# Kernel tuning notes

Measured on AMD Instinct MI355X. Metric: run time of the kernel, lower is better.

Reference implementation:

```python
import jax, jax.numpy as jnp
import numpy as np

N_NODES = 100000
N_EDGES = 1600000
N_GRAPHS = 256
BN_EPS = 1e-5


def _graph_conv(x, src, dst, ew, w_rel, b_rel, w_root):
    # PyG GraphConv: aggregate add of edge_weight * x[src] at dst, then dense transform
    msg = x[src] * ew[:, None]                      # [E, F] gathered messages
    agg = jax.ops.segment_sum(msg, dst, num_segments=N_NODES)  # [N, F]
    return agg @ w_rel + b_rel + x @ w_root


def _bn_eval(x, g, b, m, v):
    return (x - m) * jax.lax.rsqrt(v + BN_EPS) * g + b


def setup_inputs() -> dict:
    key = jax.random.key(0)
    ks = jax.random.split(key, 32)
    d = {}
    d["x"] = jax.random.normal(ks[0], (N_NODES, 29), dtype=jnp.float32)
    d["edge_index"] = jax.random.randint(ks[1], (2, N_EDGES), 0, N_NODES, dtype=jnp.int64)
    d["edge_weight"] = jax.random.uniform(ks[2], (N_EDGES,), dtype=jnp.float32)
    d["batch"] = jnp.sort(jax.random.randint(ks[3], (N_NODES,), 0, N_GRAPHS, dtype=jnp.int64))
    dims = [(29, 256), (256, 128), (128, 64), (64, 32)]
    for i, (fi, fo) in enumerate(dims, start=1):
        s = 1.0 / np.sqrt(fi)
        d[f"w{i}_rel"] = jax.random.uniform(ks[4 + 3 * i], (fi, fo), minval=-s, maxval=s, dtype=jnp.float32)
        d[f"b{i}_rel"] = jax.random.uniform(ks[5 + 3 * i], (fo,), minval=-s, maxval=s, dtype=jnp.float32)
        d[f"w{i}_root"] = jax.random.uniform(ks[6 + 3 * i], (fi, fo), minval=-s, maxval=s, dtype=jnp.float32)
    for j, c in enumerate([128, 64, 32], start=1):
        kb = jax.random.split(jax.random.fold_in(key, 100 + j), 4)
        d[f"bn{j}_g"] = 1.0 + 0.1 * jax.random.normal(kb[0], (c,), dtype=jnp.float32)
        d[f"bn{j}_b"] = 0.1 * jax.random.normal(kb[1], (c,), dtype=jnp.float32)
        d[f"bn{j}_m"] = 0.1 * jax.random.normal(kb[2], (c,), dtype=jnp.float32)
        d[f"bn{j}_v"] = 0.5 + jax.random.uniform(kb[3], (c,), dtype=jnp.float32)
    s = 1.0 / np.sqrt(32.0)
    d["fc_w"] = jax.random.uniform(ks[30], (32, 1), minval=-s, maxval=s, dtype=jnp.float32)
    d["fc_b"] = jax.random.uniform(ks[31], (1,), minval=-s, maxval=s, dtype=jnp.float32)
    return d


def reference(x, edge_index, edge_weight, batch,
              w1_rel, b1_rel, w1_root, w2_rel, b2_rel, w2_root,
              w3_rel, b3_rel, w3_root, w4_rel, b4_rel, w4_root,
              bn1_g, bn1_b, bn1_m, bn1_v,
              bn2_g, bn2_b, bn2_m, bn2_v,
              bn3_g, bn3_b, bn3_m, bn3_v,
              fc_w, fc_b):
    src, dst = edge_index[0], edge_index[1]
    h = jax.nn.relu(_graph_conv(x, src, dst, edge_weight, w1_rel, b1_rel, w1_root))
    h = _graph_conv(h, src, dst, edge_weight, w2_rel, b2_rel, w2_root)
    h = jax.nn.relu(_bn_eval(h, bn1_g, bn1_b, bn1_m, bn1_v))
    h = _graph_conv(h, src, dst, edge_weight, w3_rel, b3_rel, w3_root)
    h = jax.nn.relu(_bn_eval(h, bn2_g, bn2_b, bn2_m, bn2_v))
    h = _graph_conv(h, src, dst, edge_weight, w4_rel, b4_rel, w4_root)
    h = jax.nn.relu(_bn_eval(h, bn3_g, bn3_b, bn3_m, bn3_v))
    # global mean pool over graphs
    sums = jax.ops.segment_sum(h, batch, num_segments=N_GRAPHS)        # [G, 32]
    cnts = jax.ops.segment_sum(jnp.ones((h.shape[0],), h.dtype), batch, num_segments=N_GRAPHS)
    pooled = sums / jnp.maximum(cnts, 1.0)[:, None]
    return jax.nn.sigmoid(pooled @ fc_w + fc_b)                         # [G, 1]
```

## Files before the change

kernel.cpp:

```cpp
#include <hip/hip_runtime.h>
#include <math.h>

#define N_NODES 100000
#define N_EDGES 1600000
#define N_GRAPHS 256
#define BN_EPS 1e-5f

__global__ void hist_kernel(const int* __restrict__ ei, int* __restrict__ deg) {
    int e = blockIdx.x * blockDim.x + threadIdx.x;
    if (e < N_EDGES) atomicAdd(&deg[ei[N_EDGES + e]], 1);
}

__global__ void scan1_kernel(const int* __restrict__ deg, int* __restrict__ rowptr,
                             int* __restrict__ bsum) {
    __shared__ int s[256];
    int tid = threadIdx.x;
    int i = blockIdx.x * 256 + tid;
    int v = (i < N_NODES) ? deg[i] : 0;
    s[tid] = v; __syncthreads();
    for (int off = 1; off < 256; off <<= 1) {
        int t = (tid >= off) ? s[tid - off] : 0; __syncthreads();
        s[tid] += t; __syncthreads();
    }
    if (i < N_NODES) rowptr[i] = s[tid] - v;
    if (tid == 255) bsum[blockIdx.x] = s[255];
}

__global__ void scan2_kernel(int* bsum, int nb) {
    __shared__ int s[512];
    int tid = threadIdx.x;
    int v = (tid < nb) ? bsum[tid] : 0;
    s[tid] = v; __syncthreads();
    for (int off = 1; off < 512; off <<= 1) {
        int t = (tid >= off) ? s[tid - off] : 0; __syncthreads();
        s[tid] += t; __syncthreads();
    }
    if (tid < nb) bsum[tid] = s[tid] - v;
}

__global__ void scan3_kernel(int* __restrict__ rowptr, const int* __restrict__ bsum) {
    int i = blockIdx.x * 256 + threadIdx.x;
    if (i < N_NODES) rowptr[i] += bsum[blockIdx.x];
    if (i == 0) rowptr[N_NODES] = N_EDGES;
}

__global__ void scatter_kernel(const int* __restrict__ ei, const float* __restrict__ ew,
                               const int* __restrict__ rowptr, int* __restrict__ cnt,
                               int* __restrict__ ssrc, float* __restrict__ swt) {
    int e = blockIdx.x * blockDim.x + threadIdx.x;
    if (e >= N_EDGES) return;
    int dst = ei[N_EDGES + e];
    int pos = rowptr[dst] + atomicAdd(&cnt[dst], 1);
    ssrc[pos] = ei[e];
    swt[pos] = ew[e];
}

__global__ void bnprep_kernel(const float* __restrict__ v1, const float* __restrict__ v2,
                              const float* __restrict__ v3, float* __restrict__ rs) {
    int t = threadIdx.x;
    if (t < 128) rs[t] = 1.0f / sqrtf(v1[t] + BN_EPS);
    if (t < 64)  rs[128 + t] = 1.0f / sqrtf(v2[t] + BN_EPS);
    if (t < 32)  rs[192 + t] = 1.0f / sqrtf(v3[t] + BN_EPS);
}

__global__ void starts_kernel(const int* __restrict__ batch, int* __restrict__ starts) {
    int i = blockIdx.x * 256 + threadIdx.x;
    if (i >= N_NODES) return;
    int b = batch[i];
    int bp = (i == 0) ? -1 : batch[i - 1];
    for (int g = bp + 1; g <= b; ++g) starts[g] = i;
    if (i == N_NODES - 1)
        for (int g = b + 1; g <= N_GRAPHS; ++g) starts[g] = N_NODES;
}

__global__ __launch_bounds__(256) void pad_x_kernel(const float* __restrict__ x,
                                                    float* __restrict__ xp) {
    int i = blockIdx.x * 256 + threadIdx.x;
    if (i >= N_NODES * 32) return;
    int n = i >> 5, c = i & 31;
    xp[i] = (c < 29) ? x[n * 29 + c] : 0.f;
}

__global__ __launch_bounds__(256) void agg_x_kernel(const float* __restrict__ xp,
        const int* __restrict__ rowptr, const int* __restrict__ ssrc,
        const float* __restrict__ swt, float* __restrict__ agg) {
    int tid = threadIdx.x;
    int node = blockIdx.x * 32 + (tid >> 3);
    int c = (tid & 7) * 4;
    int e0 = rowptr[node], e1 = rowptr[node + 1];
    float4 acc = {0.f, 0.f, 0.f, 0.f};
    int e = e0;
    for (; e < e1 && (e & 3); ++e) {
        int s0 = ssrc[e]; float w0 = swt[e];
        float4 y0 = *(const float4*)&xp[(size_t)s0 * 32 + c];
        acc.x = fmaf(w0, y0.x, acc.x); acc.y = fmaf(w0, y0.y, acc.y);
        acc.z = fmaf(w0, y0.z, acc.z); acc.w = fmaf(w0, y0.w, acc.w);
    }
    for (; e + 4 <= e1; e += 4) {
        int4   s4 = *(const int4*)&ssrc[e];
        float4 w4 = *(const float4*)&swt[e];
        float4 y0 = *(const float4*)&xp[(size_t)s4.x * 32 + c];
        float4 y1 = *(const float4*)&xp[(size_t)s4.y * 32 + c];
        float4 y2 = *(const float4*)&xp[(size_t)s4.z * 32 + c];
        float4 y3 = *(const float4*)&xp[(size_t)s4.w * 32 + c];
        acc.x = fmaf(w4.x, y0.x, acc.x); acc.y = fmaf(w4.x, y0.y, acc.y);
        acc.z = fmaf(w4.x, y0.z, acc.z); acc.w = fmaf(w4.x, y0.w, acc.w);
        acc.x = fmaf(w4.y, y1.x, acc.x); acc.y = fmaf(w4.y, y1.y, acc.y);
        acc.z = fmaf(w4.y, y1.z, acc.z); acc.w = fmaf(w4.y, y1.w, acc.w);
        acc.x = fmaf(w4.z, y2.x, acc.x); acc.y = fmaf(w4.z, y2.y, acc.y);
        acc.z = fmaf(w4.z, y2.z, acc.z); acc.w = fmaf(w4.z, y2.w, acc.w);
        acc.x = fmaf(w4.w, y3.x, acc.x); acc.y = fmaf(w4.w, y3.y, acc.y);
        acc.z = fmaf(w4.w, y3.z, acc.z); acc.w = fmaf(w4.w, y3.w, acc.w);
    }
    for (; e < e1; ++e) {
        int s0 = ssrc[e]; float w0 = swt[e];
        float4 y0 = *(const float4*)&xp[(size_t)s0 * 32 + c];
        acc.x = fmaf(w0, y0.x, acc.x); acc.y = fmaf(w0, y0.y, acc.y);
        acc.z = fmaf(w0, y0.z, acc.z); acc.w = fmaf(w0, y0.w, acc.w);
    }
    *(float4*)&agg[(size_t)node * 32 + c] = acc;
}

__global__ __launch_bounds__(256) void dense1_kernel(const float* __restrict__ agg,
        const float* __restrict__ xp, const float* __restrict__ wrel,
        const float* __restrict__ wroot, const float* __restrict__ bias,
        float* __restrict__ out) {
    __shared__ float sA[32 * 32];
    __shared__ float sX[32 * 32];
    int tid = threadIdx.x;
    int node0 = blockIdx.x * 32;
    ((float4*)sA)[tid] = ((const float4*)(agg + (size_t)node0 * 32))[tid];
    ((float4*)sX)[tid] = ((const float4*)(xp + (size_t)node0 * 32))[tid];
    __syncthreads();
    int ct = tid & 63;
    int mg = tid >> 6;
    int c0 = ct * 4;
    float acc[8][4];
#pragma unroll
    for (int m = 0; m < 8; m++)
#pragma unroll
        for (int j = 0; j < 4; j++) acc[m][j] = 0.f;
    for (int k0 = 0; k0 < 28; k0 += 4) {
        float4 wr[4], wo[4];
#pragma unroll
        for (int j = 0; j < 4; j++) {
            wr[j] = *(const float4*)&wrel[(k0 + j) * 256 + c0];
            wo[j] = *(const float4*)&wroot[(k0 + j) * 256 + c0];
        }
#pragma unroll
        for (int m = 0; m < 8; m++) {
            float4 av = *(const float4*)&sA[(mg * 8 + m) * 32 + k0];
            float4 xv = *(const float4*)&sX[(mg * 8 + m) * 32 + k0];
            float as[4] = {av.x, av.y, av.z, av.w};
            float xs[4] = {xv.x, xv.y, xv.z, xv.w};
#pragma unroll
            for (int j = 0; j < 4; j++) {
                acc[m][0] = fmaf(as[j], wr[j].x, fmaf(xs[j], wo[j].x, acc[m][0]));
                acc[m][1] = fmaf(as[j], wr[j].y, fmaf(xs[j], wo[j].y, acc[m][1]));
                acc[m][2] = fmaf(as[j], wr[j].z, fmaf(xs[j], wo[j].z, acc[m][2]));
                acc[m][3] = fmaf(as[j], wr[j].w, fmaf(xs[j], wo[j].w, acc[m][3]));
            }
        }
    }
    {
        float4 wr = *(const float4*)&wrel[28 * 256 + c0];
        float4 wo = *(const float4*)&wroot[28 * 256 + c0];
#pragma unroll
        for (int m = 0; m < 8; m++) {
            float sa = sA[(mg * 8 + m) * 32 + 28];
            float sx = sX[(mg * 8 + m) * 32 + 28];
            acc[m][0] = fmaf(sa, wr.x, fmaf(sx, wo.x, acc[m][0]));
            acc[m][1] = fmaf(sa, wr.y, fmaf(sx, wo.y, acc[m][1]));
            acc[m][2] = fmaf(sa, wr.z, fmaf(sx, wo.z, acc[m][2]));
            acc[m][3] = fmaf(sa, wr.w, fmaf(sx, wo.w, acc[m][3]));
        }
    }
    float4 b4 = *(const float4*)&bias[c0];
#pragma unroll
    for (int m = 0; m < 8; m++) {
        int row = node0 + mg * 8 + m;
        float4 o;
        o.x = fmaxf(acc[m][0] + b4.x, 0.f);
        o.y = fmaxf(acc[m][1] + b4.y, 0.f);
        o.z = fmaxf(acc[m][2] + b4.z, 0.f);
        o.w = fmaxf(acc[m][3] + b4.w, 0.f);
        *(float4*)&out[(size_t)row * 256 + c0] = o;
    }
}

template <int K, int F, int RPM, int KC>
__global__ __launch_bounds__(256) void gemm_dual_kernel(const float* __restrict__ in,
        const float* __restrict__ wA, const float* __restrict__ wB,
        float* __restrict__ outA, float* __restrict__ outB) {
    constexpr int NT = 256;
    constexpr int CPT = 8;
    constexpr int CQ = CPT / 4;
    constexpr int NCT = 2 * F / CPT;
    constexpr int MG = NT / NCT;
    constexpr int ROWS = MG * RPM;
    constexpr int KC4 = KC / 4;
    __shared__ float s[ROWS * KC];
    int tid = threadIdx.x;
    size_t node0 = (size_t)blockIdx.x * ROWS;
    int ct = tid % NCT;
    int mg = tid / NCT;
    int c0 = ct * CPT;
    const float* W;
    float* OUT;
    int cc;
    if (c0 < F) { W = wA; OUT = outA; cc = c0; }
    else        { W = wB; OUT = outB; cc = c0 - F; }
    float acc[RPM][CPT];
#pragma unroll
    for (int m = 0; m < RPM; m++)
#pragma unroll
        for (int j = 0; j < CPT; j++) acc[m][j] = 0.f;
    const float* srow = s + (size_t)(mg * RPM) * KC;
    for (int kb = 0; kb < K; kb += KC) {
        __syncthreads();
        for (int idx = tid; idx < ROWS * KC4; idx += NT) {
            int rr = idx / KC4;
            int c4 = idx % KC4;
            *(float4*)&s[rr * KC + c4 * 4] =
                *(const float4*)&in[(node0 + rr) * K + kb + c4 * 4];
        }
        __syncthreads();
        for (int k0 = 0; k0 < KC; k0 += 4) {
            float4 wv[4][CQ];
#pragma unroll
            for (int j = 0; j < 4; j++)
#pragma unroll
                for (int q = 0; q < CQ; q++)
                    wv[j][q] = *(const float4*)&W[(kb + k0 + j) * F + cc + q * 4];
#pragma unroll
            for (int m = 0; m < RPM; m++) {
                float4 av = *(const float4*)&srow[m * KC + k0];
                float as[4] = {av.x, av.y, av.z, av.w};
#pragma unroll
                for (int j = 0; j < 4; j++) {
#pragma unroll
                    for (int q = 0; q < CQ; q++) {
                        acc[m][q * 4 + 0] = fmaf(as[j], wv[j][q].x, acc[m][q * 4 + 0]);
                        acc[m][q * 4 + 1] = fmaf(as[j], wv[j][q].y, acc[m][q * 4 + 1]);
                        acc[m][q * 4 + 2] = fmaf(as[j], wv[j][q].z, acc[m][q * 4 + 2]);
                        acc[m][q * 4 + 3] = fmaf(as[j], wv[j][q].w, acc[m][q * 4 + 3]);
                    }
                }
            }
        }
    }
#pragma unroll
    for (int m = 0; m < RPM; m++) {
        size_t row = node0 + mg * RPM + m;
#pragma unroll
        for (int q = 0; q < CQ; q++) {
            float4 o = {acc[m][q * 4 + 0], acc[m][q * 4 + 1],
                        acc[m][q * 4 + 2], acc[m][q * 4 + 3]};
            *(float4*)&OUT[row * F + cc + q * 4] = o;
        }
    }
}

template <int F>
__global__ __launch_bounds__(256) void combine_kernel(const float* __restrict__ y,
        const float* __restrict__ r, const int* __restrict__ rowptr,
        const int* __restrict__ ssrc, const float* __restrict__ swt,
        const float* __restrict__ bias, const float* __restrict__ bg,
        const float* __restrict__ bb, const float* __restrict__ bm,
        const float* __restrict__ rs, float* __restrict__ h) {
    constexpr int TPN = F / 4;
    int tid = threadIdx.x;
    int node = blockIdx.x * (256 / TPN) + tid / TPN;
    int c = (tid % TPN) * 4;
    int e0 = rowptr[node], e1 = rowptr[node + 1];
    float4 acc = {0.f, 0.f, 0.f, 0.f};
    int e = e0;
    for (; e < e1 && (e & 3); ++e) {
        int s0 = ssrc[e]; float w0 = swt[e];
        float4 y0 = *(const float4*)&y[(size_t)s0 * F + c];
        acc.x = fmaf(w0, y0.x, acc.x); acc.y = fmaf(w0, y0.y, acc.y);
        acc.z = fmaf(w0, y0.z, acc.z); acc.w = fmaf(w0, y0.w, acc.w);
    }
    for (; e + 4 <= e1; e += 4) {
        int4   s4 = *(const int4*)&ssrc[e];
        float4 w4 = *(const float4*)&swt[e];
        float4 y0 = *(const float4*)&y[(size_t)s4.x * F + c];
        float4 y1 = *(const float4*)&y[(size_t)s4.y * F + c];
        float4 y2 = *(const float4*)&y[(size_t)s4.z * F + c];
        float4 y3 = *(const float4*)&y[(size_t)s4.w * F + c];
        acc.x = fmaf(w4.x, y0.x, acc.x); acc.y = fmaf(w4.x, y0.y, acc.y);
        acc.z = fmaf(w4.x, y0.z, acc.z); acc.w = fmaf(w4.x, y0.w, acc.w);
        acc.x = fmaf(w4.y, y1.x, acc.x); acc.y = fmaf(w4.y, y1.y, acc.y);
        acc.z = fmaf(w4.y, y1.z, acc.z); acc.w = fmaf(w4.y, y1.w, acc.w);
        acc.x = fmaf(w4.z, y2.x, acc.x); acc.y = fmaf(w4.z, y2.y, acc.y);
        acc.z = fmaf(w4.z, y2.z, acc.z); acc.w = fmaf(w4.z, y2.w, acc.w);
        acc.x = fmaf(w4.w, y3.x, acc.x); acc.y = fmaf(w4.w, y3.y, acc.y);
        acc.z = fmaf(w4.w, y3.z, acc.z); acc.w = fmaf(w4.w, y3.w, acc.w);
    }
    for (; e < e1; ++e) {
        int s0 = ssrc[e]; float w0 = swt[e];
        float4 y0 = *(const float4*)&y[(size_t)s0 * F + c];
        acc.x = fmaf(w0, y0.x, acc.x); acc.y = fmaf(w0, y0.y, acc.y);
        acc.z = fmaf(w0, y0.z, acc.z); acc.w = fmaf(w0, y0.w, acc.w);
    }
    float4 bi = *(const float4*)&bias[c];
    float4 rv = *(const float4*)&r[(size_t)node * F + c];
    float4 mu = *(const float4*)&bm[c];
    float4 rq = *(const float4*)&rs[c];
    float4 gm = *(const float4*)&bg[c];
    float4 bt = *(const float4*)&bb[c];
    float4 o;
    o.x = fmaxf((acc.x + bi.x + rv.x - mu.x) * rq.x * gm.x + bt.x, 0.f);
    o.y = fmaxf((acc.y + bi.y + rv.y - mu.y) * rq.y * gm.y + bt.y, 0.f);
    o.z = fmaxf((acc.z + bi.z + rv.z - mu.z) * rq.z * gm.z + bt.z, 0.f);
    o.w = fmaxf((acc.w + bi.w + rv.w - mu.w) * rq.w * gm.w + bt.w, 0.f);
    *(float4*)&h[(size_t)node * F + c] = o;
}

__global__ __launch_bounds__(256) void pool_fc_kernel(const float* __restrict__ h4,
        const int* __restrict__ starts, const float* __restrict__ fcw,
        const float* __restrict__ fcb, float* __restrict__ out) {
    int g = blockIdx.x;
    int tid = threadIdx.x;
    int i0 = starts[g], i1 = starts[g + 1];
    int ch = tid & 31, part = tid >> 5;
    float sum = 0.f;
    for (int i = i0 + part; i < i1; i += 8) sum += h4[(size_t)i * 32 + ch];
    __shared__ float sm[8][32];
    sm[part][ch] = sum;
    __syncthreads();
    if (tid < 32) {
        float tot = 0.f;
        for (int p = 0; p < 8; p++) tot += sm[p][tid];
        float cnt = (float)(i1 - i0);
        float mean = tot / fmaxf(cnt, 1.0f);
        sm[0][tid] = mean * fcw[tid];
    }
    __syncthreads();
    if (tid == 0) {
        float z = 0.f;
        for (int c = 0; c < 32; c++) z += sm[0][c];
        z += fcb[0];
        out[g] = 1.0f / (1.0f + expf(-z));
    }
}

extern "C" void kernel_launch(void* const* d_in, const int* in_sizes, int n_in,
                              void* d_out, int out_size, void* d_ws, size_t ws_size,
                              hipStream_t stream) {
    (void)in_sizes; (void)n_in; (void)out_size; (void)ws_size;
    const float* x       = (const float*)d_in[0];
    const int*   ei      = (const int*)d_in[1];
    const float* ew      = (const float*)d_in[2];
    const int*   batch   = (const int*)d_in[3];
    const float* w1_rel  = (const float*)d_in[4];
    const float* b1      = (const float*)d_in[5];
    const float* w1_root = (const float*)d_in[6];
    const float* w2_rel  = (const float*)d_in[7];
    const float* b2      = (const float*)d_in[8];
    const float* w2_root = (const float*)d_in[9];
    const float* w3_rel  = (const float*)d_in[10];
    const float* b3      = (const float*)d_in[11];
    const float* w3_root = (const float*)d_in[12];
    const float* w4_rel  = (const float*)d_in[13];
    const float* b4      = (const float*)d_in[14];
    const float* w4_root = (const float*)d_in[15];
    const float* bn1_g = (const float*)d_in[16];
    const float* bn1_b = (const float*)d_in[17];
    const float* bn1_m = (const float*)d_in[18];
    const float* bn2_g = (const float*)d_in[20];
    const float* bn2_b = (const float*)d_in[21];
    const float* bn2_m = (const float*)d_in[22];
    const float* bn3_g = (const float*)d_in[24];
    const float* bn3_b = (const float*)d_in[25];
    const float* bn3_m = (const float*)d_in[26];
    const float* fc_w = (const float*)d_in[28];
    const float* fc_b = (const float*)d_in[29];

    char* ws = (char*)d_ws;
    int*   rowptr = (int*)(ws + 0);
    int*   cnt    = (int*)(ws + (1ull << 20));
    int*   bsum   = (int*)(ws + (2ull << 20));
    float* rs     = (float*)(ws + (2ull << 20) + (64ull << 10));
    int*   starts = (int*)(ws + (2ull << 20) + (128ull << 10));
    int*   ssrc   = (int*)(ws + (4ull << 20));
    float* swt    = (float*)(ws + (11ull << 20));
    float* bufA   = (float*)(ws + (18ull << 20));
    float* bufB   = (float*)(ws + (122ull << 20));
    float* bufC   = (float*)(ws + (174ull << 20));
    float* xp   = bufB;
    float* agg1 = bufC;

    hipMemsetAsync(cnt, 0, N_NODES * 4, stream);
    hist_kernel<<<6250, 256, 0, stream>>>(ei, cnt);
    scan1_kernel<<<391, 256, 0, stream>>>(cnt, rowptr, bsum);
    scan2_kernel<<<1, 512, 0, stream>>>(bsum, 391);
    scan3_kernel<<<391, 256, 0, stream>>>(rowptr, bsum);
    hipMemsetAsync(cnt, 0, N_NODES * 4, stream);
    scatter_kernel<<<6250, 256, 0, stream>>>(ei, ew, rowptr, cnt, ssrc, swt);
    bnprep_kernel<<<1, 128, 0, stream>>>((const float*)d_in[19], (const float*)d_in[23],
                                         (const float*)d_in[27], rs);
    starts_kernel<<<391, 256, 0, stream>>>(batch, starts);

    pad_x_kernel<<<12500, 256, 0, stream>>>(x, xp);
    agg_x_kernel<<<3125, 256, 0, stream>>>(xp, rowptr, ssrc, swt, agg1);
    dense1_kernel<<<3125, 256, 0, stream>>>(agg1, xp, w1_rel, w1_root, b1, bufA);

    gemm_dual_kernel<256, 128, 8, 64><<<1563, 256, 0, stream>>>(bufA, w2_rel, w2_root, bufB, bufC);
    combine_kernel<128><<<12500, 256, 0, stream>>>(bufB, bufC, rowptr, ssrc, swt,
                                                   b2, bn1_g, bn1_b, bn1_m, rs, bufC);

    gemm_dual_kernel<128, 64, 4, 64><<<1563, 256, 0, stream>>>(bufC, w3_rel, w3_root, bufB, bufA);
    combine_kernel<64><<<6250, 256, 0, stream>>>(bufB, bufA, rowptr, ssrc, swt,
                                                 b3, bn2_g, bn2_b, bn2_m, rs + 128, bufA);

    gemm_dual_kernel<64, 32, 4, 32><<<782, 256, 0, stream>>>(bufA, w4_rel, w4_root, bufB, bufC);
    combine_kernel<32><<<3125, 256, 0, stream>>>(bufB, bufC, rowptr, ssrc, swt,
                                                 b4, bn3_g, bn3_b, bn3_m, rs + 192, bufC);

    pool_fc_kernel<<<N_GRAPHS, 256, 0, stream>>>(bufC, starts, fc_w, fc_b, (float*)d_out);
}
```

Measured before the change: 859.6 us.

## Double-buffer shared tiles and prefetch weights in dual GEMM kernel

The dual GEMM kernel now stages input tiles through two shared-memory buffers, loading the next K-chunk into registers while computing the current one, and prefetches the next weight rows into a second register set. Each thread now computes 4 output columns instead of 8, with rows per thread raised to keep the tile covering the same nodes. The aim is to hide global-load latency and remove one barrier per chunk. In exchange it uses more shared memory and staging registers, which may lower occupancy.

Measured after the change: 816.0 us. 5.1% less time.

```diff
diff --git a/kernel.cpp b/kernel.cpp
--- a/kernel.cpp
+++ b/kernel.cpp
@@ -193,71 +193,102 @@
         const float* __restrict__ wA, const float* __restrict__ wB,
         float* __restrict__ outA, float* __restrict__ outB) {
     constexpr int NT = 256;
-    constexpr int CPT = 8;
-    constexpr int CQ = CPT / 4;
-    constexpr int NCT = 2 * F / CPT;
+    constexpr int NCT = F / 2;
     constexpr int MG = NT / NCT;
     constexpr int ROWS = MG * RPM;
     constexpr int KC4 = KC / 4;
-    __shared__ float s[ROWS * KC];
+    constexpr int LPT = (ROWS * KC4) / NT;
+    __shared__ float sbuf[2][ROWS * KC];
     int tid = threadIdx.x;
     size_t node0 = (size_t)blockIdx.x * ROWS;
     int ct = tid % NCT;
     int mg = tid / NCT;
-    int c0 = ct * CPT;
+    int c0 = ct * 4;
     const float* W;
     float* OUT;
     int cc;
     if (c0 < F) { W = wA; OUT = outA; cc = c0; }
     else        { W = wB; OUT = outB; cc = c0 - F; }
-    float acc[RPM][CPT];
+    float acc[RPM][4];
 #pragma unroll
     for (int m = 0; m < RPM; m++)
 #pragma unroll
-        for (int j = 0; j < CPT; j++) acc[m][j] = 0.f;
-    const float* srow = s + (size_t)(mg * RPM) * KC;
+        for (int j = 0; j < 4; j++) acc[m][j] = 0.f;
+
+#pragma unroll
+    for (int i = 0; i < LPT; i++) {
+        int idx = tid + i * NT;
+        int rr = idx / KC4, c4 = idx % KC4;
+        *(float4*)&sbuf[0][rr * KC + c4 * 4] =
+            *(const float4*)&in[(node0 + rr) * K + c4 * 4];
+    }
+    float4 wv[2][4];
+#pragma unroll
+    for (int j = 0; j < 4; j++) wv[0][j] = *(const float4*)&W[j * F + cc];
+    __syncthreads();
+
+    int cur = 0;
+#pragma unroll 1
     for (int kb = 0; kb < K; kb += KC) {
-        __syncthreads();
-        for (int idx = tid; idx < ROWS * KC4; idx += NT) {
-            int rr = idx / KC4;
-            int c4 = idx % KC4;
-            *(float4*)&s[rr * KC + c4 * 4] =
-                *(const float4*)&in[(node0 + rr) * K + kb + c4 * 4];
-        }
-        __syncthreads();
+        const bool more = (kb + KC < K);
+        float4 st[LPT];
+        if (more) {
+#pragma unroll
+            for (int i = 0; i < LPT; i++) {
+                int idx = tid + i * NT;
+                int rr = idx / KC4, c4 = idx % KC4;
+                st[i] = *(const float4*)&in[(node0 + rr) * K + (kb + KC) + c4 * 4];
+            }
+        }
+        const float* srow = &sbuf[cur][0] + (size_t)(mg * RPM) * KC;
+#pragma unroll
         for (int k0 = 0; k0 < KC; k0 += 4) {
-            float4 wv[4][CQ];
-#pragma unroll
-            for (int j = 0; j < 4; j++)
-#pragma unroll
-                for (int q = 0; q < CQ; q++)
-                    wv[j][q] = *(const float4*)&W[(kb + k0 + j) * F + cc + q * 4];
+            const int pf = (k0 / 4) & 1;
+            const int nx = pf ^ 1;
+            int kn = kb + k0 + 4;
+            if (kn < K) {
+#pragma unroll
+                for (int j = 0; j < 4; j++)
+                    wv[nx][j] = *(const float4*)&W[(size_t)(kn + j) * F + cc];
+            }
 #pragma unroll
             for (int m = 0; m < RPM; m++) {
-                float4 av = *(const float4*)&srow[m * KC + k0];
-                float as[4] = {av.x, av.y, av.z, av.w};
-#pragma unroll
-                for (int j = 0; j < 4; j++) {
-#pragma unroll
-                    for (int q = 0; q < CQ; q++) {
-                        acc[m][q * 4 + 0] = fmaf(as[j], wv[j][q].x, acc[m][q * 4 + 0]);
-                        acc[m][q * 4 + 1] = fmaf(as[j], wv[j][q].y, acc[m][q * 4 + 1]);
-                        acc[m][q * 4 + 2] = fmaf(as[j], wv[j][q].z, acc[m][q * 4 + 2]);
-                        acc[m][q * 4 + 3] = fmaf(as[j], wv[j][q].w, acc[m][q * 4 + 3]);
-                    }
-                }
+                float4 sm = *(const float4*)&srow[m * KC + k0];
+                acc[m][0] = fmaf(sm.x, wv[pf][0].x, acc[m][0]);
+                acc[m][1] = fmaf(sm.x, wv[pf][0].y, acc[m][1]);
+                acc[m][2] = fmaf(sm.x, wv[pf][0].z, acc[m][2]);
+                acc[m][3] = fmaf(sm.x, wv[pf][0].w, acc[m][3]);
+                acc[m][0] = fmaf(sm.y, wv[pf][1].x, acc[m][0]);
+                acc[m][1] = fmaf(sm.y, wv[pf][1].y, acc[m][1]);
+                acc[m][2] = fmaf(sm.y, wv[pf][1].z, acc[m][2]);
+                acc[m][3] = fmaf(sm.y, wv[pf][1].w, acc[m][3]);
+                acc[m][0] = fmaf(sm.z, wv[pf][2].x, acc[m][0]);
+                acc[m][1] = fmaf(sm.z, wv[pf][2].y, acc[m][1]);
+                acc[m][2] = fmaf(sm.z, wv[pf][2].z, acc[m][2]);
+                acc[m][3] = fmaf(sm.z, wv[pf][2].w, acc[m][3]);
+                acc[m][0] = fmaf(sm.w, wv[pf][3].x, acc[m][0]);
+                acc[m][1] = fmaf(sm.w, wv[pf][3].y, acc[m][1]);
+                acc[m][2] = fmaf(sm.w, wv[pf][3].z, acc[m][2]);
+                acc[m][3] = fmaf(sm.w, wv[pf][3].w, acc[m][3]);
             }
+        }
+        if (more) {
+            float* dbuf = &sbuf[cur ^ 1][0];
+#pragma unroll
+            for (int i = 0; i < LPT; i++) {
+                int idx = tid + i * NT;
+                int rr = idx / KC4, c4 = idx % KC4;
+                *(float4*)&dbuf[rr * KC + c4 * 4] = st[i];
+            }
+            cur ^= 1;
+            __syncthreads();
         }
     }
 #pragma unroll
     for (int m = 0; m < RPM; m++) {
         size_t row = node0 + mg * RPM + m;
-#pragma unroll
-        for (int q = 0; q < CQ; q++) {
-            float4 o = {acc[m][q * 4 + 0], acc[m][q * 4 + 1],
-                        acc[m][q * 4 + 2], acc[m][q * 4 + 3]};
-            *(float4*)&OUT[row * F + cc + q * 4] = o;
-        }
+        float4 o = {acc[m][0], acc[m][1], acc[m][2], acc[m][3]};
+        *(float4*)&OUT[row * F + cc] = o;
     }
 }
 
@@ -406,15 +437,15 @@
     agg_x_kernel<<<3125, 256, 0, stream>>>(xp, rowptr, ssrc, swt, agg1);
     dense1_kernel<<<3125, 256, 0, stream>>>(agg1, xp, w1_rel, w1_root, b1, bufA);
 
-    gemm_dual_kernel<256, 128, 8, 64><<<1563, 256, 0, stream>>>(bufA, w2_rel, w2_root, bufB, bufC);
+    gemm_dual_kernel<256, 128, 16, 64><<<1563, 256, 0, stream>>>(bufA, w2_rel, w2_root, bufB, bufC);
     combine_kernel<128><<<12500, 256, 0, stream>>>(bufB, bufC, rowptr, ssrc, swt,
                                                    b2, bn1_g, bn1_b, bn1_m, rs, bufC);
 
-    gemm_dual_kernel<128, 64, 4, 64><<<1563, 256, 0, stream>>>(bufC, w3_rel, w3_root, bufB, bufA);
+    gemm_dual_kernel<128, 64, 8, 64><<<1563, 256, 0, stream>>>(bufC, w3_rel, w3_root, bufB, bufA);
     combine_kernel<64><<<6250, 256, 0, stream>>>(bufB, bufA, rowptr, ssrc, swt,
                                                  b3, bn2_g, bn2_b, bn2_m, rs + 128, bufA);
 
-    gemm_dual_kernel<64, 32, 4, 32><<<782, 256, 0, stream>>>(bufA, w4_rel, w4_root, bufB, bufC);
+    gemm_dual_kernel<64, 32, 4, 32><<<1563, 256, 0, stream>>>(bufA, w4_rel, w4_root, bufB, bufC);
     combine_kernel<32><<<3125, 256, 0, stream>>>(bufB, bufC, rowptr, ssrc, swt,
                                                  b4, bn3_g, bn3_b, bn3_m, rs + 192, bufC);
 
```
